# Optimization experiments

Measured on AMD Instinct MI355X. Metric: run time of the kernel, lower is better.

## Reference

```python
import jax, jax.numpy as jnp
import numpy as np

B, S, D_IN, D_MODEL = 4, 2048, 1024, 1024


def setup_inputs() -> dict:
    key = jax.random.key(0)
    ks = jax.random.split(key, 8)
    glorot = np.sqrt(6.0 / (D_IN + D_MODEL))
    inp = {
        "q": jax.random.normal(ks[0], (B, S, D_IN), dtype=jnp.float32),
        "k": jax.random.normal(ks[1], (B, S, D_IN), dtype=jnp.float32),
        "v": jax.random.normal(ks[2], (B, S, D_IN), dtype=jnp.float32),
        "mask": jnp.zeros((1, S, S), dtype=jnp.float32),
        # conv kernels with shape (1, look_back=1, d_in, d_model)
        "kernel_q": jax.random.uniform(ks[3], (1, 1, D_IN, D_MODEL), jnp.float32, -glorot, glorot),
        "kernel_k": jax.random.uniform(ks[4], (1, 1, D_IN, D_MODEL), jnp.float32, -glorot, glorot),
        "kernel_v": jax.random.uniform(ks[5], (1, 1, D_IN, D_MODEL), jnp.float32, -glorot, glorot),
        "bias_q": 0.05 * jax.random.normal(ks[6], (D_MODEL,), dtype=jnp.float32),
        "bias_k": 0.05 * jax.random.normal(ks[7], (D_MODEL,), dtype=jnp.float32),
        "bias_v": 0.05 * jax.random.normal(jax.random.fold_in(key, 7), (D_MODEL,), dtype=jnp.float32),
    }
    return inp


def reference(q, k, v, mask, kernel_q, kernel_k, kernel_v, bias_q, bias_k, bias_v):
    # look_back == 1: the (1,1,d_in,d_model) conv is a per-token linear projection.
    Wq, Wk, Wv = kernel_q[0, 0], kernel_k[0, 0], kernel_v[0, 0]  # [d_in, d_model]
    qp = jax.nn.relu(jnp.einsum("bsd,de->bse", q, Wq) + bias_q)  # [B,S,D]
    kp = jax.nn.relu(jnp.einsum("bsd,de->bse", k, Wk) + bias_k)
    vp = jax.nn.relu(jnp.einsum("bsd,de->bse", v, Wv) + bias_v)
    # unnormalized relu-attention: relu(QK^T)/sqrt(dk) + mask (no softmax)
    scores = jax.nn.relu(jnp.einsum("bqe,bke->bqk", qp, kp))  # [B,S,S]
    dk = jnp.asarray(kp.shape[-1], dtype=scores.dtype)
    logits = scores / jnp.sqrt(dk) + mask
    out = jax.nn.relu(jnp.einsum("bqk,bke->bqe", logits, vp))  # [B,S,D]
    return out
```

## Files before the change

kernel.cpp:

```cpp
#include <hip/hip_runtime.h>


#define B_ 4
#define S_ 2048
#define D_ 1024

typedef __attribute__((ext_vector_type(8))) short short8;
typedef __attribute__((ext_vector_type(4))) float f32x4;
typedef const __attribute__((address_space(1))) void* gas1;
typedef __attribute__((address_space(3))) void* las3;

template <int V> struct IC { static constexpr int value = V; };

static __device__ __forceinline__ short f2bf(float x) {
    union { float f; unsigned u; } un; un.f = x;
    unsigned r = un.u + 0x7fff + ((un.u >> 16) & 1);
    return (short)(r >> 16);
}

__global__ void cvt3_kernel(const float* __restrict__ q, const float* __restrict__ k,
                            const float* __restrict__ v, short* __restrict__ out) {
    const float* in = (blockIdx.y == 0) ? q : ((blockIdx.y == 1) ? k : v);
    size_t i = ((size_t)blockIdx.x * blockDim.x + threadIdx.x) * 8;
    short* o = out + (size_t)blockIdx.y * ((size_t)B_ * S_ * D_);
    float4 a = *(const float4*)(in + i);
    float4 b = *(const float4*)(in + i + 4);
    short8 r;
    r[0] = f2bf(a.x); r[1] = f2bf(a.y); r[2] = f2bf(a.z); r[3] = f2bf(a.w);
    r[4] = f2bf(b.x); r[5] = f2bf(b.y); r[6] = f2bf(b.z); r[7] = f2bf(b.w);
    *(short8*)(o + i) = r;
}

__global__ void make_wT_kernel(const float* __restrict__ Wq, const float* __restrict__ Wk,
                               const float* __restrict__ Wv, short* __restrict__ wT) {
    const float* W = (blockIdx.z == 0) ? Wq : ((blockIdx.z == 1) ? Wk : Wv);
    short* o = wT + (size_t)blockIdx.z * D_ * D_;
    __shared__ float t[32][33];
    int bx = blockIdx.x, by = blockIdx.y;
    int tx = threadIdx.x & 31, ty = threadIdx.x >> 5;
    #pragma unroll
    for (int r = ty; r < 32; r += 8)
        t[r][tx] = W[(size_t)(by * 32 + r) * D_ + bx * 32 + tx];
    __syncthreads();
    #pragma unroll
    for (int r = ty; r < 32; r += 8)
        o[(size_t)(bx * 32 + r) * D_ + by * 32 + tx] = f2bf(t[tx][r]);
}

__global__ void transpose_bf16_kernel(const short* __restrict__ in, short* __restrict__ out) {
    __shared__ short t[64][65];
    int b = blockIdx.z;
    int e0 = blockIdx.x * 64, s0 = blockIdx.y * 64;
    const short* src = in + (size_t)b * S_ * D_;
    short* dst = out + (size_t)b * D_ * S_;
    int tx = threadIdx.x & 63, ty = threadIdx.x >> 6;
    #pragma unroll
    for (int r = ty; r < 64; r += 4)
        t[r][tx] = src[(size_t)(s0 + r) * D_ + e0 + tx];
    __syncthreads();
    #pragma unroll
    for (int r = ty; r < 64; r += 4)
        dst[(size_t)(e0 + r) * S_ + s0 + tx] = t[tx][r];
}

template <int M_REP, int N_REP, int EPI>
__global__ __launch_bounds__(512, 2)
void gemm8p_kernel(const short* __restrict__ A, const short* __restrict__ B, void* __restrict__ Cv,
                   int K, int lda, int ldb, int ldc,
                   size_t sA, size_t sB, size_t sC,
                   const float* __restrict__ bias0, const float* __restrict__ bias1,
                   const float* __restrict__ bias2,
                   const float* __restrict__ mask, int ldmask) {
    constexpr int BM = 32 * M_REP;
    constexpr int BN = 64 * N_REP;
    constexpr int A_LOADS = BM / 128;
    constexpr int B_LOADS = BN / 128;
    constexpr int VMN = 2 * B_LOADS;

    __shared__ short As[2][BM * 64];
    __shared__ short Bs[2][BN * 64];

    const int gx = gridDim.x, gy = gridDim.y;
    const int nwg = gx * gy * gridDim.z;
    const int flat = blockIdx.x + gx * (blockIdx.y + gy * blockIdx.z);
    const int swz = (flat & 7) * (nwg >> 3) + (flat >> 3);
    const int bx = swz % gx;
    const int rem = swz / gx;
    const int by = rem % gy;
    const int bz = rem / gy;

    const int m0 = bx * BM, n0 = by * BN;
    const short* Ab = A + (size_t)bz * sA;
    const short* Bb = B + (size_t)bz * sB;

    const int tid = threadIdx.x;
    const int lane = tid & 63;
    const int w = tid >> 6;
    const int wr = w >> 2, wc = w & 3;
    const int lr16 = lane & 15, kq = lane >> 4;
    const int NT = K >> 6;

    const int csrc = (((lane & 7) ^ (lane >> 3)) << 3);

    auto stageA = [&](int par, int half, int kt) {
        if (kt >= NT) return;
        #pragma unroll
        for (int l = 0; l < A_LOADS; ++l) {
            int chunk = w * A_LOADS + l;
            int row = half * (BM / 2) + chunk * 8 + (lane >> 3);
            const short* src = Ab + (size_t)(m0 + row) * lda + kt * 64 + csrc;
            las3 dst = (las3)&As[par][half * (BM / 2) * 64 + chunk * 512 + lane * 8];
            __builtin_amdgcn_global_load_lds((gas1)src, dst, 16, 0, 0);
        }
    };
    auto stageB = [&](int par, int half, int kt) {
        if (kt >= NT) return;
        #pragma unroll
        for (int l = 0; l < B_LOADS; ++l) {
            int chunk = w * B_LOADS + l;
            int row = half * (BN / 2) + chunk * 8 + (lane >> 3);
            const short* src = Bb + (size_t)(n0 + row) * ldb + kt * 64 + csrc;
            las3 dst = (las3)&Bs[par][half * (BN / 2) * 64 + chunk * 512 + lane * 8];
            __builtin_amdgcn_global_load_lds((gas1)src, dst, 16, 0, 0);
        }
    };
    auto ldA = [&](int par, int m, int ks) -> short8 {
        int row = wr * (BM / 2) + m * 16 + lr16;
        int col = (ks * 32 + kq * 8) ^ ((lr16 & 7) * 8);
        return *(const short8*)&As[par][row * 64 + col];
    };
    auto ldB = [&](int par, int n, int ks) -> short8 {
        int row = wc * (16 * N_REP) + n * 16 + lr16;
        int col = (ks * 32 + kq * 8) ^ ((lr16 & 7) * 8);
        return *(const short8*)&Bs[par][row * 64 + col];
    };

    f32x4 acc[M_REP][N_REP] = {};
    short8 bfr[2][N_REP];

    stageA(0, 0, 0); stageA(0, 1, 0);
    stageB(0, 0, 0); stageB(0, 1, 0);
    stageB(1, 0, 1); stageB(1, 1, 1);
    if constexpr (VMN == 4) asm volatile("s_waitcnt vmcnt(4)" ::: "memory");
    else                    asm volatile("s_waitcnt vmcnt(2)" ::: "memory");
    __builtin_amdgcn_s_barrier();

    auto phase = [&](int par, auto ksC, auto mhC, auto stage, auto vmC) {
        constexpr int ks = decltype(ksC)::value;
        constexpr int mh = decltype(mhC)::value;
        constexpr int vm = decltype(vmC)::value;
        short8 a[M_REP / 2];
        #pragma unroll
        for (int m = 0; m < M_REP / 2; ++m) a[m] = ldA(par, mh * (M_REP / 2) + m, ks);
        if constexpr (mh == 0) {
            #pragma unroll
            for (int n = 0; n < N_REP; ++n) bfr[ks][n] = ldB(par, n, ks);
        }
        stage();
        __builtin_amdgcn_s_barrier();
        asm volatile("s_waitcnt lgkmcnt(0)" ::: "memory");
        __builtin_amdgcn_sched_barrier(0);
        __builtin_amdgcn_s_setprio(1);
        #pragma unroll
        for (int m = 0; m < M_REP / 2; ++m)
            #pragma unroll
            for (int n = 0; n < N_REP; ++n)
                acc[mh * (M_REP / 2) + m][n] =
                    __builtin_amdgcn_mfma_f32_16x16x32_bf16(a[m], bfr[ks][n],
                                                            acc[mh * (M_REP / 2) + m][n], 0, 0, 0);
        __builtin_amdgcn_s_setprio(0);
        if constexpr (vm) {
            if constexpr (VMN == 4) asm volatile("s_waitcnt vmcnt(4)" ::: "memory");
            else                    asm volatile("s_waitcnt vmcnt(2)" ::: "memory");
        }
        __builtin_amdgcn_s_barrier();
    };

    #pragma unroll 1
    for (int I = 0; I < (NT >> 1); ++I) {
        const int t1 = 2 * I + 1, t2 = 2 * I + 2, t3 = 2 * I + 3;
        phase(0, IC<0>{}, IC<0>{}, [&] { stageA(1, 0, t1); }, IC<0>{});
        phase(0, IC<1>{}, IC<0>{}, [&] { stageA(1, 1, t1); }, IC<0>{});
        phase(0, IC<0>{}, IC<1>{}, [&] { stageB(0, 0, t2); }, IC<0>{});
        phase(0, IC<1>{}, IC<1>{}, [&] { stageB(0, 1, t2); }, IC<1>{});
        phase(1, IC<0>{}, IC<0>{}, [&] { stageA(0, 0, t2); }, IC<0>{});
        phase(1, IC<1>{}, IC<0>{}, [&] { stageA(0, 1, t2); }, IC<0>{});
        phase(1, IC<0>{}, IC<1>{}, [&] { stageB(1, 0, t3); }, IC<0>{});
        phase(1, IC<1>{}, IC<1>{}, [&] { stageB(1, 1, t3); }, IC<1>{});
    }
    asm volatile("s_waitcnt vmcnt(0)" ::: "memory");

    short* Cs = (short*)Cv + (size_t)bz * sC;
    float* Cf = (float*)Cv + (size_t)bz * sC;
    const float* bias = (EPI == 0) ? ((bz == 0) ? bias0 : ((bz == 1) ? bias1 : bias2)) : nullptr;
    #pragma unroll
    for (int mi = 0; mi < M_REP; ++mi) {
        #pragma unroll
        for (int ni = 0; ni < N_REP; ++ni) {
            int n = n0 + wc * (16 * N_REP) + ni * 16 + lr16;
            int mb = m0 + wr * (BM / 2) + mi * 16 + kq * 4;
            #pragma unroll
            for (int j = 0; j < 4; ++j) {
                int m = mb + j;
                float val = acc[mi][ni][j];
                if constexpr (EPI == 0) {
                    val = fmaxf(val + bias[n], 0.f);
                    Cs[(size_t)m * ldc + n] = f2bf(val);
                } else if constexpr (EPI == 1) {
                    val = fmaxf(val, 0.f) * 0.03125f + mask[(size_t)m * ldmask + n];
                    Cs[(size_t)m * ldc + n] = f2bf(val);
                } else {
                    Cf[(size_t)m * ldc + n] = fmaxf(val, 0.f);
                }
            }
        }
    }
}

extern "C" void kernel_launch(void* const* d_in, const int* in_sizes, int n_in,
                              void* d_out, int out_size, void* d_ws, size_t ws_size,
                              hipStream_t stream) {
    const float* q    = (const float*)d_in[0];
    const float* k    = (const float*)d_in[1];
    const float* v    = (const float*)d_in[2];
    const float* mask = (const float*)d_in[3];
    const float* Wq   = (const float*)d_in[4];
    const float* Wk   = (const float*)d_in[5];
    const float* Wv   = (const float*)d_in[6];
    const float* bq   = (const float*)d_in[7];
    const float* bk   = (const float*)d_in[8];
    const float* bv   = (const float*)d_in[9];
    float* out = (float*)d_out;

    char* ws = (char*)d_ws;
    short* wT     = (short*)(ws);
    short* qkv_bf = (short*)(ws + 6291456);
    short* logits = (short*)(ws + 6291456);
    short* qkvp   = (short*)(ws + 56623104);
    short* qp     = qkvp;
    short* kp     = qkvp + (size_t)B_ * S_ * D_;
    short* vp     = qkvp + 2 * (size_t)B_ * S_ * D_;
    short* vpT    = qp;

    const size_t tok = (size_t)B_ * S_;
    const size_t tokD = tok * D_;

    make_wT_kernel<<<dim3(32, 32, 3), 256, 0, stream>>>(Wq, Wk, Wv, wT);

    cvt3_kernel<<<dim3(tokD / 8 / 256, 3), 256, 0, stream>>>(q, k, v, qkv_bf);

    gemm8p_kernel<8, 2, 0><<<dim3(32, 8, 3), 512, 0, stream>>>(
        qkv_bf, wT, qkvp, D_, D_, D_, D_,
        tokD, (size_t)D_ * D_, tokD, bq, bk, bv, nullptr, 0);

    gemm8p_kernel<8, 4, 1><<<dim3(8, 8, 4), 512, 0, stream>>>(
        qp, kp, logits, D_, D_, D_, S_,
        (size_t)S_ * D_, (size_t)S_ * D_, (size_t)S_ * S_,
        nullptr, nullptr, nullptr, mask, S_);

    transpose_bf16_kernel<<<dim3(D_ / 64, S_ / 64, B_), 256, 0, stream>>>(vp, vpT);

    gemm8p_kernel<8, 2, 2><<<dim3(8, 8, 4), 512, 0, stream>>>(
        logits, vpT, out, S_, S_, S_, D_,
        (size_t)S_ * S_, (size_t)D_ * S_, (size_t)S_ * D_,
        nullptr, nullptr, nullptr, nullptr, 0);
}
```

Before: 360.5 us.

## Replace 8-phase K=64 GEMM pipeline with 4-phase K=32 double-buffered loop

Rewrites the bf16 MFMA GEMM to stage 32-wide K slices instead of 64, halving LDS footprint per buffer. It uses a new XOR swizzle and configurable warp grids (WM x WN), and raises launch bounds to allow 4 blocks per CU. The pipeline becomes a simpler 4-phase loop that drains all outstanding loads every half-iteration, trading prefetch depth and fine-grained overlap for occupancy and fewer barriers per tile. Block swizzle order is also changed to walk N first within a strip.

New measurement: 576.8 us. 60.0% more time.

```diff
diff --git a/kernel.cpp b/kernel.cpp
--- a/kernel.cpp
+++ b/kernel.cpp
@@ -63,31 +63,30 @@
         dst[(size_t)(e0 + r) * S_ + s0 + tx] = t[tx][r];
 }
 
-template <int M_REP, int N_REP, int EPI>
-__global__ __launch_bounds__(512, 2)
-void gemm8p_kernel(const short* __restrict__ A, const short* __restrict__ B, void* __restrict__ Cv,
+template <int M_REP, int N_REP, int WM, int WN, int EPI>
+__global__ __launch_bounds__(512, 4)
+void gemm4p_kernel(const short* __restrict__ A, const short* __restrict__ B, void* __restrict__ Cv,
                    int K, int lda, int ldb, int ldc,
                    size_t sA, size_t sB, size_t sC,
                    const float* __restrict__ bias0, const float* __restrict__ bias1,
                    const float* __restrict__ bias2,
                    const float* __restrict__ mask, int ldmask) {
-    constexpr int BM = 32 * M_REP;
-    constexpr int BN = 64 * N_REP;
-    constexpr int A_LOADS = BM / 128;
-    constexpr int B_LOADS = BN / 128;
-    constexpr int VMN = 2 * B_LOADS;
-
-    __shared__ short As[2][BM * 64];
-    __shared__ short Bs[2][BN * 64];
-
-    const int gx = gridDim.x, gy = gridDim.y;
-    const int nwg = gx * gy * gridDim.z;
-    const int flat = blockIdx.x + gx * (blockIdx.y + gy * blockIdx.z);
-    const int swz = (flat & 7) * (nwg >> 3) + (flat >> 3);
-    const int bx = swz % gx;
-    const int rem = swz / gx;
-    const int by = rem % gy;
-    const int bz = rem / gy;
+    constexpr int BM = 16 * M_REP * WM;
+    constexpr int BN = 16 * N_REP * WN;
+    constexpr int AR = (BM * 32 * 2) / 8192;
+    constexpr int BR = (BN * 32 * 2) / 8192;
+
+    __shared__ short As[2][BM * 32];
+    __shared__ short Bs[2][BN * 32];
+
+    const int GX = gridDim.x, GY = gridDim.y;
+    const int nwg = GX * GY * gridDim.z;
+    const int flat = blockIdx.x + GX * (blockIdx.y + GY * blockIdx.z);
+    const int g = (flat & 7) * (nwg >> 3) + (flat >> 3);
+    const int by = g % GY;
+    const int strip = g / GY;
+    const int bx = strip % GX;
+    const int bz = strip / GX;
 
     const int m0 = bx * BM, n0 = by * BN;
     const short* Ab = A + (size_t)bz * sA;
@@ -96,67 +95,59 @@
     const int tid = threadIdx.x;
     const int lane = tid & 63;
     const int w = tid >> 6;
-    const int wr = w >> 2, wc = w & 3;
+    const int wc = w % WN, wr = w / WN;
     const int lr16 = lane & 15, kq = lane >> 4;
-    const int NT = K >> 6;
-
-    const int csrc = (((lane & 7) ^ (lane >> 3)) << 3);
-
-    auto stageA = [&](int par, int half, int kt) {
+    const int NT = K >> 5;
+
+    const int csrc = (((tid & 3) ^ ((tid >> 3) & 3)) << 3);
+
+    auto stageA = [&](int par, int kt) {
         if (kt >= NT) return;
         #pragma unroll
-        for (int l = 0; l < A_LOADS; ++l) {
-            int chunk = w * A_LOADS + l;
-            int row = half * (BM / 2) + chunk * 8 + (lane >> 3);
-            const short* src = Ab + (size_t)(m0 + row) * lda + kt * 64 + csrc;
-            las3 dst = (las3)&As[par][half * (BM / 2) * 64 + chunk * 512 + lane * 8];
-            __builtin_amdgcn_global_load_lds((gas1)src, dst, 16, 0, 0);
-        }
-    };
-    auto stageB = [&](int par, int half, int kt) {
+        for (int R = 0; R < AR; ++R) {
+            int row = R * 128 + (tid >> 2);
+            const short* src = Ab + (size_t)(m0 + row) * lda + kt * 32 + csrc;
+            __builtin_amdgcn_global_load_lds((gas1)src, (las3)&As[par][R * 4096 + tid * 8], 16, 0, 0);
+        }
+    };
+    auto stageB = [&](int par, int kt) {
         if (kt >= NT) return;
         #pragma unroll
-        for (int l = 0; l < B_LOADS; ++l) {
-            int chunk = w * B_LOADS + l;
-            int row = half * (BN / 2) + chunk * 8 + (lane >> 3);
-            const short* src = Bb + (size_t)(n0 + row) * ldb + kt * 64 + csrc;
-            las3 dst = (las3)&Bs[par][half * (BN / 2) * 64 + chunk * 512 + lane * 8];
-            __builtin_amdgcn_global_load_lds((gas1)src, dst, 16, 0, 0);
-        }
-    };
-    auto ldA = [&](int par, int m, int ks) -> short8 {
-        int row = wr * (BM / 2) + m * 16 + lr16;
-        int col = (ks * 32 + kq * 8) ^ ((lr16 & 7) * 8);
-        return *(const short8*)&As[par][row * 64 + col];
-    };
-    auto ldB = [&](int par, int n, int ks) -> short8 {
-        int row = wc * (16 * N_REP) + n * 16 + lr16;
-        int col = (ks * 32 + kq * 8) ^ ((lr16 & 7) * 8);
-        return *(const short8*)&Bs[par][row * 64 + col];
+        for (int R = 0; R < BR; ++R) {
+            int row = R * 128 + (tid >> 2);
+            const short* src = Bb + (size_t)(n0 + row) * ldb + kt * 32 + csrc;
+            __builtin_amdgcn_global_load_lds((gas1)src, (las3)&Bs[par][R * 4096 + tid * 8], 16, 0, 0);
+        }
+    };
+    auto ldA = [&](int par, int mi) -> short8 {
+        int row = wr * (16 * M_REP) + mi * 16 + lr16;
+        int col = (kq ^ ((row >> 1) & 3)) << 3;
+        return *(const short8*)&As[par][row * 32 + col];
+    };
+    auto ldB = [&](int par, int ni) -> short8 {
+        int row = wc * (16 * N_REP) + ni * 16 + lr16;
+        int col = (kq ^ ((row >> 1) & 3)) << 3;
+        return *(const short8*)&Bs[par][row * 32 + col];
     };
 
     f32x4 acc[M_REP][N_REP] = {};
-    short8 bfr[2][N_REP];
-
-    stageA(0, 0, 0); stageA(0, 1, 0);
-    stageB(0, 0, 0); stageB(0, 1, 0);
-    stageB(1, 0, 1); stageB(1, 1, 1);
-    if constexpr (VMN == 4) asm volatile("s_waitcnt vmcnt(4)" ::: "memory");
-    else                    asm volatile("s_waitcnt vmcnt(2)" ::: "memory");
+    short8 bfr[N_REP];
+
+    stageA(0, 0); stageB(0, 0);
+    asm volatile("s_waitcnt vmcnt(0)" ::: "memory");
     __builtin_amdgcn_s_barrier();
 
-    auto phase = [&](int par, auto ksC, auto mhC, auto stage, auto vmC) {
-        constexpr int ks = decltype(ksC)::value;
+    auto phase = [&](int par, auto mhC, auto stageF, auto drainC) {
         constexpr int mh = decltype(mhC)::value;
-        constexpr int vm = decltype(vmC)::value;
+        constexpr int drain = decltype(drainC)::value;
         short8 a[M_REP / 2];
         #pragma unroll
-        for (int m = 0; m < M_REP / 2; ++m) a[m] = ldA(par, mh * (M_REP / 2) + m, ks);
+        for (int m = 0; m < M_REP / 2; ++m) a[m] = ldA(par, mh * (M_REP / 2) + m);
         if constexpr (mh == 0) {
             #pragma unroll
-            for (int n = 0; n < N_REP; ++n) bfr[ks][n] = ldB(par, n, ks);
-        }
-        stage();
+            for (int n = 0; n < N_REP; ++n) bfr[n] = ldB(par, n);
+        }
+        stageF();
         __builtin_amdgcn_s_barrier();
         asm volatile("s_waitcnt lgkmcnt(0)" ::: "memory");
         __builtin_amdgcn_sched_barrier(0);
@@ -166,29 +157,20 @@
             #pragma unroll
             for (int n = 0; n < N_REP; ++n)
                 acc[mh * (M_REP / 2) + m][n] =
-                    __builtin_amdgcn_mfma_f32_16x16x32_bf16(a[m], bfr[ks][n],
+                    __builtin_amdgcn_mfma_f32_16x16x32_bf16(a[m], bfr[n],
                                                             acc[mh * (M_REP / 2) + m][n], 0, 0, 0);
         __builtin_amdgcn_s_setprio(0);
-        if constexpr (vm) {
-            if constexpr (VMN == 4) asm volatile("s_waitcnt vmcnt(4)" ::: "memory");
-            else                    asm volatile("s_waitcnt vmcnt(2)" ::: "memory");
-        }
+        if constexpr (drain) asm volatile("s_waitcnt vmcnt(0)" ::: "memory");
         __builtin_amdgcn_s_barrier();
     };
 
     #pragma unroll 1
     for (int I = 0; I < (NT >> 1); ++I) {
-        const int t1 = 2 * I + 1, t2 = 2 * I + 2, t3 = 2 * I + 3;
-        phase(0, IC<0>{}, IC<0>{}, [&] { stageA(1, 0, t1); }, IC<0>{});
-        phase(0, IC<1>{}, IC<0>{}, [&] { stageA(1, 1, t1); }, IC<0>{});
-        phase(0, IC<0>{}, IC<1>{}, [&] { stageB(0, 0, t2); }, IC<0>{});
-        phase(0, IC<1>{}, IC<1>{}, [&] { stageB(0, 1, t2); }, IC<1>{});
-        phase(1, IC<0>{}, IC<0>{}, [&] { stageA(0, 0, t2); }, IC<0>{});
-        phase(1, IC<1>{}, IC<0>{}, [&] { stageA(0, 1, t2); }, IC<0>{});
-        phase(1, IC<0>{}, IC<1>{}, [&] { stageB(1, 0, t3); }, IC<0>{});
-        phase(1, IC<1>{}, IC<1>{}, [&] { stageB(1, 1, t3); }, IC<1>{});
+        phase(0, IC<0>{}, [&] { stageA(1, 2 * I + 1); stageB(1, 2 * I + 1); }, IC<0>{});
+        phase(0, IC<1>{}, [&] {}, IC<1>{});
+        phase(1, IC<0>{}, [&] { stageA(0, 2 * I + 2); stageB(0, 2 * I + 2); }, IC<0>{});
+        phase(1, IC<1>{}, [&] {}, IC<1>{});
     }
-    asm volatile("s_waitcnt vmcnt(0)" ::: "memory");
 
     short* Cs = (short*)Cv + (size_t)bz * sC;
     float* Cf = (float*)Cv + (size_t)bz * sC;
@@ -198,7 +180,7 @@
         #pragma unroll
         for (int ni = 0; ni < N_REP; ++ni) {
             int n = n0 + wc * (16 * N_REP) + ni * 16 + lr16;
-            int mb = m0 + wr * (BM / 2) + mi * 16 + kq * 4;
+            int mb = m0 + wr * (16 * M_REP) + mi * 16 + kq * 4;
             #pragma unroll
             for (int j = 0; j < 4; ++j) {
                 int m = mb + j;
@@ -249,18 +231,18 @@
 
     cvt3_kernel<<<dim3(tokD / 8 / 256, 3), 256, 0, stream>>>(q, k, v, qkv_bf);
 
-    gemm8p_kernel<8, 2, 0><<<dim3(32, 8, 3), 512, 0, stream>>>(
+    gemm4p_kernel<4, 4, 4, 2, 0><<<dim3(32, 8, 3), 512, 0, stream>>>(
         qkv_bf, wT, qkvp, D_, D_, D_, D_,
         tokD, (size_t)D_ * D_, tokD, bq, bk, bv, nullptr, 0);
 
-    gemm8p_kernel<8, 4, 1><<<dim3(8, 8, 4), 512, 0, stream>>>(
+    gemm4p_kernel<8, 4, 2, 4, 1><<<dim3(8, 8, 4), 512, 0, stream>>>(
         qp, kp, logits, D_, D_, D_, S_,
         (size_t)S_ * D_, (size_t)S_ * D_, (size_t)S_ * S_,
         nullptr, nullptr, nullptr, mask, S_);
 
     transpose_bf16_kernel<<<dim3(D_ / 64, S_ / 64, B_), 256, 0, stream>>>(vp, vpT);
 
-    gemm8p_kernel<8, 2, 2><<<dim3(8, 8, 4), 512, 0, stream>>>(
+    gemm4p_kernel<4, 4, 4, 2, 2><<<dim3(8, 8, 4), 512, 0, stream>>>(
         logits, vpT, out, S_, S_, S_, D_,
         (size_t)S_ * S_, (size_t)D_ * S_, (size_t)S_ * D_,
         nullptr, nullptr, nullptr, nullptr, 0);
```

## Restructure GEMM pipeline into four fused phases with a peeled final iteration

Applied to the files above, without the earlier changes.

Each main-loop phase now handles both k-substeps (ks=0 and ks=1), so the loop runs four phases instead of eight. This halves the barrier count per iteration and batches more LDS reads before each MFMA burst. Tile staging is rewritten to issue whole-tile loads with one flat per-thread mapping, and the last iteration is peeled with explicit vmcnt(0) handling so no out-of-range guards are needed. The cost is higher register pressure from holding two k-substeps of A/B fragments, and the scheduling barrier before the MFMAs is removed.

Measured after the change: 353.6 us. No clear change (-1.9%).

```diff
diff --git a/kernel.cpp b/kernel.cpp
--- a/kernel.cpp
+++ b/kernel.cpp
@@ -65,17 +65,17 @@
 
 template <int M_REP, int N_REP, int EPI>
 __global__ __launch_bounds__(512, 2)
-void gemm8p_kernel(const short* __restrict__ A, const short* __restrict__ B, void* __restrict__ Cv,
+void gemmf4_kernel(const short* __restrict__ A, const short* __restrict__ B, void* __restrict__ Cv,
                    int K, int lda, int ldb, int ldc,
                    size_t sA, size_t sB, size_t sC,
                    const float* __restrict__ bias0, const float* __restrict__ bias1,
                    const float* __restrict__ bias2,
                    const float* __restrict__ mask, int ldmask) {
-    constexpr int BM = 32 * M_REP;
-    constexpr int BN = 64 * N_REP;
-    constexpr int A_LOADS = BM / 128;
-    constexpr int B_LOADS = BN / 128;
-    constexpr int VMN = 2 * B_LOADS;
+    constexpr int BM = 16 * M_REP * 2;
+    constexpr int BN = 16 * N_REP * 4;
+    constexpr int AR = BM / 64;
+    constexpr int BR = BN / 64;
+    constexpr int VMN = BR * 1;
 
     __shared__ short As[2][BM * 64];
     __shared__ short Bs[2][BN * 64];
@@ -100,37 +100,31 @@
     const int lr16 = lane & 15, kq = lane >> 4;
     const int NT = K >> 6;
 
-    const int csrc = (((lane & 7) ^ (lane >> 3)) << 3);
-
-    auto stageA = [&](int par, int half, int kt) {
-        if (kt >= NT) return;
-        #pragma unroll
-        for (int l = 0; l < A_LOADS; ++l) {
-            int chunk = w * A_LOADS + l;
-            int row = half * (BM / 2) + chunk * 8 + (lane >> 3);
+    const int csrc = (((tid & 7) ^ ((tid >> 3) & 7)) << 3);
+
+    auto stageA = [&](int par, int kt) {
+        #pragma unroll
+        for (int R = 0; R < AR; ++R) {
+            int row = R * 64 + (tid >> 3);
             const short* src = Ab + (size_t)(m0 + row) * lda + kt * 64 + csrc;
-            las3 dst = (las3)&As[par][half * (BM / 2) * 64 + chunk * 512 + lane * 8];
-            __builtin_amdgcn_global_load_lds((gas1)src, dst, 16, 0, 0);
-        }
-    };
-    auto stageB = [&](int par, int half, int kt) {
-        if (kt >= NT) return;
-        #pragma unroll
-        for (int l = 0; l < B_LOADS; ++l) {
-            int chunk = w * B_LOADS + l;
-            int row = half * (BN / 2) + chunk * 8 + (lane >> 3);
+            __builtin_amdgcn_global_load_lds((gas1)src, (las3)&As[par][R * 4096 + tid * 8], 16, 0, 0);
+        }
+    };
+    auto stageB = [&](int par, int kt) {
+        #pragma unroll
+        for (int R = 0; R < BR; ++R) {
+            int row = R * 64 + (tid >> 3);
             const short* src = Bb + (size_t)(n0 + row) * ldb + kt * 64 + csrc;
-            las3 dst = (las3)&Bs[par][half * (BN / 2) * 64 + chunk * 512 + lane * 8];
-            __builtin_amdgcn_global_load_lds((gas1)src, dst, 16, 0, 0);
-        }
-    };
-    auto ldA = [&](int par, int m, int ks) -> short8 {
-        int row = wr * (BM / 2) + m * 16 + lr16;
+            __builtin_amdgcn_global_load_lds((gas1)src, (las3)&Bs[par][R * 4096 + tid * 8], 16, 0, 0);
+        }
+    };
+    auto ldA = [&](int par, int mi, int ks) -> short8 {
+        int row = wr * (BM / 2) + mi * 16 + lr16;
         int col = (ks * 32 + kq * 8) ^ ((lr16 & 7) * 8);
         return *(const short8*)&As[par][row * 64 + col];
     };
-    auto ldB = [&](int par, int n, int ks) -> short8 {
-        int row = wc * (16 * N_REP) + n * 16 + lr16;
+    auto ldB = [&](int par, int ni, int ks) -> short8 {
+        int row = wc * (16 * N_REP) + ni * 16 + lr16;
         int col = (ks * 32 + kq * 8) ^ ((lr16 & 7) * 8);
         return *(const short8*)&Bs[par][row * 64 + col];
     };
@@ -138,57 +132,62 @@
     f32x4 acc[M_REP][N_REP] = {};
     short8 bfr[2][N_REP];
 
-    stageA(0, 0, 0); stageA(0, 1, 0);
-    stageB(0, 0, 0); stageB(0, 1, 0);
-    stageB(1, 0, 1); stageB(1, 1, 1);
+    stageA(0, 0); stageB(0, 0); stageB(1, 1);
     if constexpr (VMN == 4) asm volatile("s_waitcnt vmcnt(4)" ::: "memory");
     else                    asm volatile("s_waitcnt vmcnt(2)" ::: "memory");
     __builtin_amdgcn_s_barrier();
 
-    auto phase = [&](int par, auto ksC, auto mhC, auto stage, auto vmC) {
-        constexpr int ks = decltype(ksC)::value;
+    auto fphase = [&](int par, auto mhC, auto stageF, auto vmC) {
         constexpr int mh = decltype(mhC)::value;
-        constexpr int vm = decltype(vmC)::value;
-        short8 a[M_REP / 2];
-        #pragma unroll
-        for (int m = 0; m < M_REP / 2; ++m) a[m] = ldA(par, mh * (M_REP / 2) + m, ks);
+        constexpr int vmMode = decltype(vmC)::value;
+        short8 a[2][M_REP / 2];
+        #pragma unroll
+        for (int ks = 0; ks < 2; ++ks)
+            #pragma unroll
+            for (int m = 0; m < M_REP / 2; ++m)
+                a[ks][m] = ldA(par, mh * (M_REP / 2) + m, ks);
         if constexpr (mh == 0) {
             #pragma unroll
-            for (int n = 0; n < N_REP; ++n) bfr[ks][n] = ldB(par, n, ks);
-        }
-        stage();
+            for (int ks = 0; ks < 2; ++ks)
+                #pragma unroll
+                for (int n = 0; n < N_REP; ++n)
+                    bfr[ks][n] = ldB(par, n, ks);
+        }
+        stageF();
         __builtin_amdgcn_s_barrier();
         asm volatile("s_waitcnt lgkmcnt(0)" ::: "memory");
-        __builtin_amdgcn_sched_barrier(0);
         __builtin_amdgcn_s_setprio(1);
         #pragma unroll
-        for (int m = 0; m < M_REP / 2; ++m)
-            #pragma unroll
-            for (int n = 0; n < N_REP; ++n)
-                acc[mh * (M_REP / 2) + m][n] =
-                    __builtin_amdgcn_mfma_f32_16x16x32_bf16(a[m], bfr[ks][n],
-                                                            acc[mh * (M_REP / 2) + m][n], 0, 0, 0);
+        for (int ks = 0; ks < 2; ++ks)
+            #pragma unroll
+            for (int m = 0; m < M_REP / 2; ++m)
+                #pragma unroll
+                for (int n = 0; n < N_REP; ++n)
+                    acc[mh * (M_REP / 2) + m][n] =
+                        __builtin_amdgcn_mfma_f32_16x16x32_bf16(a[ks][m], bfr[ks][n],
+                                                                acc[mh * (M_REP / 2) + m][n], 0, 0, 0);
         __builtin_amdgcn_s_setprio(0);
-        if constexpr (vm) {
+        if constexpr (vmMode == 1) {
             if constexpr (VMN == 4) asm volatile("s_waitcnt vmcnt(4)" ::: "memory");
             else                    asm volatile("s_waitcnt vmcnt(2)" ::: "memory");
+        } else if constexpr (vmMode == 2) {
+            asm volatile("s_waitcnt vmcnt(0)" ::: "memory");
         }
         __builtin_amdgcn_s_barrier();
     };
 
     #pragma unroll 1
-    for (int I = 0; I < (NT >> 1); ++I) {
+    for (int I = 0; I < (NT >> 1) - 1; ++I) {
         const int t1 = 2 * I + 1, t2 = 2 * I + 2, t3 = 2 * I + 3;
-        phase(0, IC<0>{}, IC<0>{}, [&] { stageA(1, 0, t1); }, IC<0>{});
-        phase(0, IC<1>{}, IC<0>{}, [&] { stageA(1, 1, t1); }, IC<0>{});
-        phase(0, IC<0>{}, IC<1>{}, [&] { stageB(0, 0, t2); }, IC<0>{});
-        phase(0, IC<1>{}, IC<1>{}, [&] { stageB(0, 1, t2); }, IC<1>{});
-        phase(1, IC<0>{}, IC<0>{}, [&] { stageA(0, 0, t2); }, IC<0>{});
-        phase(1, IC<1>{}, IC<0>{}, [&] { stageA(0, 1, t2); }, IC<0>{});
-        phase(1, IC<0>{}, IC<1>{}, [&] { stageB(1, 0, t3); }, IC<0>{});
-        phase(1, IC<1>{}, IC<1>{}, [&] { stageB(1, 1, t3); }, IC<1>{});
+        fphase(0, IC<0>{}, [&] { stageA(1, t1); }, IC<0>{});
+        fphase(0, IC<1>{}, [&] { stageB(0, t2); }, IC<1>{});
+        fphase(1, IC<0>{}, [&] { stageA(0, t2); }, IC<0>{});
+        fphase(1, IC<1>{}, [&] { stageB(1, t3); }, IC<1>{});
     }
-    asm volatile("s_waitcnt vmcnt(0)" ::: "memory");
+    fphase(0, IC<0>{}, [&] { stageA(1, NT - 1); }, IC<0>{});
+    fphase(0, IC<1>{}, [&] {}, IC<2>{});
+    fphase(1, IC<0>{}, [&] {}, IC<0>{});
+    fphase(1, IC<1>{}, [&] {}, IC<0>{});
 
     short* Cs = (short*)Cv + (size_t)bz * sC;
     float* Cf = (float*)Cv + (size_t)bz * sC;
@@ -249,18 +248,18 @@
 
     cvt3_kernel<<<dim3(tokD / 8 / 256, 3), 256, 0, stream>>>(q, k, v, qkv_bf);
 
-    gemm8p_kernel<8, 2, 0><<<dim3(32, 8, 3), 512, 0, stream>>>(
+    gemmf4_kernel<8, 2, 0><<<dim3(32, 8, 3), 512, 0, stream>>>(
         qkv_bf, wT, qkvp, D_, D_, D_, D_,
         tokD, (size_t)D_ * D_, tokD, bq, bk, bv, nullptr, 0);
 
-    gemm8p_kernel<8, 4, 1><<<dim3(8, 8, 4), 512, 0, stream>>>(
+    gemmf4_kernel<8, 4, 1><<<dim3(8, 8, 4), 512, 0, stream>>>(
         qp, kp, logits, D_, D_, D_, S_,
         (size_t)S_ * D_, (size_t)S_ * D_, (size_t)S_ * S_,
         nullptr, nullptr, nullptr, mask, S_);
 
     transpose_bf16_kernel<<<dim3(D_ / 64, S_ / 64, B_), 256, 0, stream>>>(vp, vpT);
 
-    gemm8p_kernel<8, 2, 2><<<dim3(8, 8, 4), 512, 0, stream>>>(
+    gemmf4_kernel<8, 2, 2><<<dim3(8, 8, 4), 512, 0, stream>>>(
         logits, vpT, out, S_, S_, S_, D_,
         (size_t)S_ * S_, (size_t)D_ * S_, (size_t)S_ * D_,
         nullptr, nullptr, nullptr, nullptr, 0);
```
